# Performance work log

Hardware: AMD Instinct MI355X
Metric: run time of the kernel (lower is better)

The kernel has to match this reference:

```python
import jax, jax.numpy as jnp
import numpy as np

DIM = 1024
VOCAB = 32000
NSEQ = 32
LENGTHS = 64 - np.arange(NSEQ) // 2  # descending seq lengths 64..49 (packed seqs are length-sorted)


def setup_inputs() -> dict:
    key = jax.random.key(0)
    k1, k2, k3, k4, k5 = jax.random.split(key, 5)
    T = int(LENGTHS.max())
    batch_sizes = np.array([(LENGTHS > t).sum() for t in range(T)], dtype=np.int32)
    total = int(batch_sizes.sum())  # 1808 packed tokens
    hidden_states = jax.random.normal(k1, (total, 2 * DIM), dtype=jnp.float32)
    sentences = jax.random.randint(k2, (total,), 0, VOCAB, dtype=jnp.int32)
    weight = jax.random.normal(k3, (VOCAB, DIM), dtype=jnp.float32) * (1.0 / np.sqrt(DIM))
    fwd_bias = jax.random.normal(k4, (VOCAB,), dtype=jnp.float32) * 0.01
    bwd_bias = jax.random.normal(k5, (VOCAB,), dtype=jnp.float32) * 0.01
    return {
        "hidden_states": hidden_states,
        "weight": weight,
        "fwd_bias": fwd_bias,
        "bwd_bias": bwd_bias,
        "sentences": sentences,
        "batch_sizes": jnp.asarray(batch_sizes),
    }


def _build_indices(batch_sizes):
    # Static (host-side) index construction replicating the per-timestep Python loops.
    bs = np.asarray(batch_sizes)
    off = np.concatenate([[0], np.cumsum(bs)])  # start row of each timestep block
    T = len(bs)
    # forward: hidden at t-1 (first bs[t] rows) predicts token at t
    ctx_f = np.concatenate([off[t - 1] + np.arange(bs[t]) for t in range(1, T)])
    tgt_f = np.concatenate([off[t] + np.arange(bs[t]) for t in range(1, T)])
    # backward: hidden at i+1 predicts token at i (first bs[i+1] rows), i = T-2 .. 1
    ctx_b = np.concatenate([off[i + 1] + np.arange(bs[i + 1]) for i in range(1, T - 1)])
    tgt_b = np.concatenate([off[i] + np.arange(bs[i + 1]) for i in range(1, T - 1)])
    denom = float(2 * bs.sum() - bs[0] - bs[-1])
    return ctx_f, tgt_f, ctx_b, tgt_b, denom


def _ce_sum(h, W, b, tgt):
    # sum-reduced cross entropy: one fused GEMM over all packed rows
    logits = h @ W.T + b  # [N, V]
    lse = jax.nn.logsumexp(logits, axis=-1)  # [N]
    gold = jnp.take_along_axis(logits, tgt[:, None], axis=1)[:, 0]  # [N]
    return jnp.sum(lse - gold)


def reference(hidden_states, weight, fwd_bias, bwd_bias, sentences, batch_sizes):
    dim = hidden_states.shape[1] // 2
    ctx_f, tgt_f, ctx_b, tgt_b, denom = _build_indices(batch_sizes)
    loss_f = _ce_sum(hidden_states[ctx_f, :dim], weight, fwd_bias, sentences[tgt_f])
    loss_b = _ce_sum(hidden_states[ctx_b, dim:], weight, bwd_bias, sentences[tgt_b])
    return (loss_f + loss_b) / denom
```

## Files before the change

### kernel.cpp

```cpp
#include <hip/hip_runtime.h>
#include <hip/hip_bf16.h>
#include <stdint.h>

typedef float f32x16 __attribute__((ext_vector_type(16)));
typedef int   i32x4  __attribute__((ext_vector_type(4)));
typedef int   i32x8  __attribute__((ext_vector_type(8)));

#define LOG2E 1.4426950408889634f
#define WSCALE 16.0f
#define AS1 __attribute__((address_space(1)))
#define AS3 __attribute__((address_space(3)))


__device__ __forceinline__ uint32_t f32_to_e4m3(float x) {
    uint32_t ux = __float_as_uint(x);
    uint32_t s = (ux >> 24) & 0x80u;
    float a = __uint_as_float(ux & 0x7FFFFFFFu);
    if (a >= 448.0f) return s | 0x7Eu;
    int e = (int)((ux >> 23) & 0xFFu) - 127;
    if (e < -6) {
        int n = __float2int_rn(a * 512.0f);
        return s | (uint32_t)n;
    }
    uint32_t m = ux & 0x7FFFFFu;
    uint32_t r = (m + 0x7FFFFu + ((m >> 20) & 1u)) >> 20;
    if (r == 8u) { r = 0u; e += 1; }
    if (e > 8 || (e == 8 && r == 7u)) return s | 0x7Eu;
    return s | ((uint32_t)(e + 7) << 3) | r;
}

__device__ __forceinline__ uint32_t pack4_fp8v(float4 v, float sc) {
    return f32_to_e4m3(v.x * sc) | (f32_to_e4m3(v.y * sc) << 8) |
           (f32_to_e4m3(v.z * sc) << 16) | (f32_to_e4m3(v.w * sc) << 24);
}

__device__ __forceinline__ uint32_t pack4_fp8(const float* s, float sc) {
    return f32_to_e4m3(s[0] * sc) | (f32_to_e4m3(s[1] * sc) << 8) |
           (f32_to_e4m3(s[2] * sc) << 16) | (f32_to_e4m3(s[3] * sc) << 24);
}

__device__ __forceinline__ uint4 cvt16_fp8(const float* s, float sc) {
    uint4 r;
    r.x = pack4_fp8(s, sc);      r.y = pack4_fp8(s + 4, sc);
    r.z = pack4_fp8(s + 8, sc);  r.w = pack4_fp8(s + 12, sc);
    return r;
}

__global__ void prep_kernel(const int* __restrict__ bs, int T,
                            const int* __restrict__ sentences,
                            int* __restrict__ hdr, float* __restrict__ fhdr,
                            int* __restrict__ row_ctx, int* __restrict__ row_tok) {
    __shared__ int off[1025];
    if (threadIdx.x == 0) {
        int acc = 0; off[0] = 0;
        for (int t = 0; t < T; ++t) { acc += bs[t]; off[t + 1] = acc; }
    }
    __syncthreads();
    const int total = off[T];
    const int Nf = total - off[1];
    const int Nb = total - off[2];
    for (int t = 1; t < T; ++t) {
        int start = off[t] - off[1];
        int cnt = off[t + 1] - off[t];
        for (int p = threadIdx.x; p < cnt; p += blockDim.x) {
            row_ctx[start + p] = off[t - 1] + p;
            row_tok[start + p] = sentences[off[t] + p];
        }
    }
    for (int i = 1; i < T - 1; ++i) {
        int start = Nf + off[i + 1] - off[2];
        int cnt = off[i + 2] - off[i + 1];
        for (int p = threadIdx.x; p < cnt; p += blockDim.x) {
            row_ctx[start + p] = off[i + 1] + p;
            row_tok[start + p] = sentences[off[i] + p];
        }
    }
    if (threadIdx.x == 0) {
        hdr[0] = Nf + Nb;
        hdr[1] = Nf;
        int bs0 = off[1];
        int bsl = off[T] - off[T - 1];
        fhdr[0] = (float)(2 * total - bs0 - bsl);
    }
}

__global__ void wconv_kernel(const float* __restrict__ W,
                             uint8_t* __restrict__ Wb, int K) {
    const int p = blockIdx.x >> 3, f = blockIdx.x & 7;
    __shared__ __align__(16) char tile[2048];
    char* panel = (char*)Wb + (size_t)p * ((size_t)K << 8);
    const int tid = threadIdx.x;
    const int rloc = tid >> 4;
    const int kloc = (tid & 15) << 2;
    const int h = (kloc >> 4) & 1;
    const int l = ((kloc >> 5) << 5) | rloc;
    const int ldst = h * 1024 + l * 16 + (kloc & 15);
    const float* src = W + (size_t)(p * 256 + f * 32 + rloc) * K + kloc;
    const int NT = K >> 6;
    for (int t = 0; t < NT; ++t) {
        const float4 v = *(const float4*)(src + t * 64);
        const uint32_t pk = pack4_fp8v(v, WSCALE);
        __syncthreads();
        *(uint32_t*)(tile + ldst) = pk;
        __syncthreads();
        if (tid < 128)
            *(uint4*)(panel + (size_t)t * 16384 + f * 2048 + (tid << 4)) =
                *(const uint4*)(tile + (tid << 4));
    }
}

__global__ void gather_kernel(const float* __restrict__ hs,
                              const int* __restrict__ row_ctx,
                              const int* __restrict__ hdr,
                              uint8_t* __restrict__ Hc,
                              float* __restrict__ S, int D2, int K) {
    const int p = blockIdx.x >> 2, f = blockIdx.x & 3;
    const int M = hdr[0], Nf = hdr[1];
    if (f == 0 && threadIdx.x < 128) S[p * 128 + threadIdx.x] = 0.f;
    char* panel = (char*)Hc + (size_t)p * ((size_t)K << 7);
    const int row0 = p * 128 + f * 32;
    const int nch = (K >> 6) << 7;
    for (int c = threadIdx.x; c < nch; c += 512) {
        const int t = c >> 7, h = (c >> 6) & 1, l = c & 63;
        const int row = row0 + (l & 31);
        char* d = panel + (size_t)t * 8192 + f * 2048 + h * 1024 + l * 16;
        if (row >= M) {
            uint4 z; z.x = z.y = z.z = z.w = 0u;
            *(uint4*)d = z;
        } else {
            const int ctx = row_ctx[row];
            const int k = t * 64 + ((l >> 5) << 5) + h * 16;
            *(uint4*)d = cvt16_fp8(hs + (size_t)ctx * D2 + (row < Nf ? 0 : K) + k, 1.0f);
        }
    }
}

__device__ __forceinline__ i32x8 ld_frag(const char* base) {
    i32x4 lo = *(const i32x4*)(base);
    i32x4 hi = *(const i32x4*)(base + 1024);
    i32x8 r;
    r[0] = lo[0]; r[1] = lo[1]; r[2] = lo[2]; r[3] = lo[3];
    r[4] = hi[0]; r[5] = hi[1]; r[6] = hi[2]; r[7] = hi[3];
    return r;
}

__global__ __launch_bounds__(512, 4)
void gemm_lse(const uint8_t* __restrict__ A,
              const uint8_t* __restrict__ B,
              const float* __restrict__ fb,
              const float* __restrict__ bb,
              float* __restrict__ S,
              const int* __restrict__ hdr, int K, int MT) {
    const int M = hdr[0], Nf = hdr[1];

    const int nwg = gridDim.x, orig = blockIdx.x;
    const int q = nwg >> 3, rr = nwg & 7;
    const int xcd = orig & 7, i8 = orig >> 3;
    const int wgid = (xcd < rr ? xcd * (q + 1) : rr * (q + 1) + (xcd - rr) * q) + i8;
    const int bm = wgid % MT, bn = wgid / MT;
    if (bm * 128 >= M) return;

    __shared__ __align__(16) char lA[2][8192];
    __shared__ __align__(16) char lB[2][16384];

    const int tid = threadIdx.x, lane = tid & 63, wid = tid >> 6;
    const int wm = wid >> 2, wn = wid & 3;

    f32x16 acc00 = (f32x16)0.f, acc01 = (f32x16)0.f;
    f32x16 acc10 = (f32x16)0.f, acc11 = (f32x16)0.f;

    const char* Ap = (const char*)A + (size_t)bm * ((size_t)K << 7);
    const char* Bp = (const char*)B + (size_t)bn * ((size_t)K << 8);
    const int sd = tid << 4;
    const int ao = ((wm * 2) << 11) + (lane << 4);
    const int bo = ((wn * 2) << 11) + (lane << 4);

#define GLDS(src, dst) __builtin_amdgcn_global_load_lds(                      \
        (const AS1 uint32_t*)(src), (AS3 uint32_t*)(dst), 16, 0, 0)

#define STAGE(buf, s) do {                                                    \
    GLDS(Ap + ((size_t)(s) << 13) + sd,        lA[buf] + sd);                 \
    GLDS(Bp + ((size_t)(s) << 14) + sd,        lB[buf] + sd);                 \
    GLDS(Bp + ((size_t)(s) << 14) + 8192 + sd, lB[buf] + 8192 + sd);          \
} while (0)

#define COMPUTE(buf) do {                                                     \
    i32x8 a0 = ld_frag(lA[buf] + ao);                                         \
    i32x8 a1 = ld_frag(lA[buf] + ao + 2048);                                  \
    i32x8 b0 = ld_frag(lB[buf] + bo);                                         \
    i32x8 b1 = ld_frag(lB[buf] + bo + 2048);                                  \
    __builtin_amdgcn_s_setprio(1);                                            \
    acc00 = __builtin_amdgcn_mfma_scale_f32_32x32x64_f8f6f4(                  \
        a0, b0, acc00, 0, 0, 0, 127, 0, 127);                                 \
    acc01 = __builtin_amdgcn_mfma_scale_f32_32x32x64_f8f6f4(                  \
        a0, b1, acc01, 0, 0, 0, 127, 0, 127);                                 \
    acc10 = __builtin_amdgcn_mfma_scale_f32_32x32x64_f8f6f4(                  \
        a1, b0, acc10, 0, 0, 0, 127, 0, 127);                                 \
    acc11 = __builtin_amdgcn_mfma_scale_f32_32x32x64_f8f6f4(                  \
        a1, b1, acc11, 0, 0, 0, 127, 0, 127);                                 \
    __builtin_amdgcn_s_setprio(0);                                            \
} while (0)

#define BAR() do { __builtin_amdgcn_s_barrier(); __builtin_amdgcn_sched_barrier(0); } while (0)

    const int NT = K >> 6;

    STAGE(0, 0);
    for (int t = 0; t < NT - 1; ++t) {
        STAGE((t + 1) & 1, t + 1);
        asm volatile("s_waitcnt vmcnt(3)" ::: "memory");
        BAR();
        COMPUTE(t & 1);
        BAR();
    }
    asm volatile("s_waitcnt vmcnt(0)" ::: "memory");
    BAR();
    COMPUTE((NT - 1) & 1);

    const float k1 = LOG2E / WSCALE;
    const int v0 = bn * 256 + wn * 64 + (lane & 31);
    const float fbv0 = fb[v0] * LOG2E,      bbv0 = bb[v0] * LOG2E;
    const float fbv1 = fb[v0 + 32] * LOG2E, bbv1 = bb[v0 + 32] * LOG2E;
    const int mb0 = bm * 128 + wm * 64 + ((lane >> 5) << 2);

#define EPI(T0, T1, MB) do {                                                  \
    _Pragma("unroll")                                                         \
    for (int reg = 0; reg < 16; ++reg) {                                      \
        const int m = (MB) + (reg & 3) + ((reg >> 2) << 3);                   \
        if (m < M) {            \
            const bool isf = m < Nf;                                          \
            float ps = exp2f(fmaf(T0[reg], k1, isf ? fbv0 : bbv0))            \
                     + exp2f(fmaf(T1[reg], k1, isf ? fbv1 : bbv1));           \
            _Pragma("unroll")                                                 \
            for (int s = 1; s < 32; s <<= 1) ps += __shfl_xor(ps, s);         \
            if ((lane & 31) == 0) atomicAdd(&S[m], ps);                       \
        }                                                                     \
    }                                                                         \
} while (0)

    EPI(acc00, acc01, mb0);
    EPI(acc10, acc11, mb0 + 32);

#undef GLDS
#undef STAGE
#undef COMPUTE
#undef BAR
#undef EPI
}

__global__ void lse_naive(const float* __restrict__ hs,
                          const float* __restrict__ W,
                          const float* __restrict__ fb,
                          const float* __restrict__ bb,
                          const int* __restrict__ row_ctx,
                          const int* __restrict__ hdr,
                          float* __restrict__ S, int D2, int D, int V) {
    const int m = blockIdx.x;
    const int M = hdr[0], Nf = hdr[1];
    if (m >= M) return;
    __shared__ float hrow[2048];
    const int ctx = row_ctx[m];
    const float* h = hs + (size_t)ctx * D2 + (m < Nf ? 0 : D);
    for (int i = threadIdx.x; i < D; i += blockDim.x) hrow[i] = h[i];
    __syncthreads();
    const float* bias = (m < Nf) ? fb : bb;
    float ps = 0.f;
    for (int v = threadIdx.x; v < V; v += blockDim.x) {
        const float* w = W + (size_t)v * D;
        float dot = 0.f;
        for (int k = 0; k < D; ++k) dot = fmaf(hrow[k], w[k], dot);
        ps += exp2f((dot + bias[v]) * LOG2E);
    }
#pragma unroll
    for (int d = 1; d < 64; d <<= 1) ps += __shfl_xor(ps, d);
    __shared__ float wsum[4];
    const int wid = threadIdx.x >> 6, lane = threadIdx.x & 63;
    if (lane == 0) wsum[wid] = ps;
    __syncthreads();
    if (threadIdx.x == 0) S[m] = wsum[0] + wsum[1] + wsum[2] + wsum[3];
}

__global__ void gold_kernel(const float* __restrict__ hs,
                            const float* __restrict__ W,
                            const float* __restrict__ fb,
                            const float* __restrict__ bb,
                            const int* __restrict__ row_ctx,
                            const int* __restrict__ row_tok,
                            const int* __restrict__ hdr,
                            float* __restrict__ goldv, int D2, int D) {
    const int m = blockIdx.x;
    const int M = hdr[0];
    if (m >= M) return;
    const int Nf = hdr[1];
    const int ctx = row_ctx[m], tok = row_tok[m];
    const float4* h = (const float4*)(hs + (size_t)ctx * D2 + (m < Nf ? 0 : D));
    const float4* w = (const float4*)(W + (size_t)tok * D);
    float s = 0.f;
    for (int i = threadIdx.x; i < D / 4; i += blockDim.x) {
        float4 a = h[i], b = w[i];
        s += a.x * b.x + a.y * b.y + a.z * b.z + a.w * b.w;
    }
#pragma unroll
    for (int d = 1; d < 64; d <<= 1) s += __shfl_xor(s, d);
    __shared__ float wsum[4];
    const int wid = threadIdx.x >> 6, lane = threadIdx.x & 63;
    if (lane == 0) wsum[wid] = s;
    __syncthreads();
    if (threadIdx.x == 0) {
        float tot = wsum[0] + wsum[1] + wsum[2] + wsum[3];
        tot += (m < Nf ? fb[tok] : bb[tok]);
        goldv[m] = tot;
    }
}

__global__ void final_kernel(const float* __restrict__ S,
                             const float* __restrict__ goldv,
                             const int* __restrict__ hdr,
                             const float* __restrict__ fhdr,
                             float* __restrict__ out) {
    const int M = hdr[0];
    float s = 0.f;
    for (int m = threadIdx.x; m < M; m += blockDim.x)
        s += logf(S[m]) - goldv[m];
#pragma unroll
    for (int d = 1; d < 64; d <<= 1) s += __shfl_xor(s, d);
    __shared__ float wsum[4];
    const int wid = threadIdx.x >> 6, lane = threadIdx.x & 63;
    if (lane == 0) wsum[wid] = s;
    __syncthreads();
    if (threadIdx.x == 0)
        out[0] = (wsum[0] + wsum[1] + wsum[2] + wsum[3]) / fhdr[0];
}

extern "C" void kernel_launch(void* const* d_in, const int* in_sizes, int n_in,
                              void* d_out, int out_size, void* d_ws, size_t ws_size,
                              hipStream_t stream) {
    const float* hs  = (const float*)d_in[0];
    const float* W   = (const float*)d_in[1];
    const float* fb  = (const float*)d_in[2];
    const float* bb  = (const float*)d_in[3];
    const int* sent  = (const int*)d_in[4];
    const int* bs    = (const int*)d_in[5];
    const int total  = in_sizes[4];
    const int T      = in_sizes[5];
    const int V      = in_sizes[2];
    const int D      = in_sizes[1] / V;
    const int D2     = in_sizes[0] / total;
    const int Mcap   = ((2 * total) + 127) & ~127;
    const int MT     = Mcap / 128;
    const int NN     = V / 256;

    char* p = (char*)d_ws;
    int*   hdr     = (int*)p;            p += 256;
    float* fhdr    = (float*)p;          p += 256;
    int*   row_ctx = (int*)p;            p += (size_t)Mcap * 4;
    int*   row_tok = (int*)p;            p += (size_t)Mcap * 4;
    float* S       = (float*)p;          p += (size_t)Mcap * 4;
    float* goldv   = (float*)p;          p += (size_t)Mcap * 4;
    uint8_t* Hc    = (uint8_t*)p;        p += (size_t)Mcap * D;
    uint8_t* Wb    = (uint8_t*)p;
    const size_t need_wb = (size_t)(p - (char*)d_ws) + (size_t)V * D;

    prep_kernel<<<1, 256, 0, stream>>>(bs, T, sent, hdr, fhdr, row_ctx, row_tok);

    if (ws_size >= need_wb) {
        gather_kernel<<<MT * 4, 512, 0, stream>>>(hs, row_ctx, hdr, Hc, S, D2, D);
        wconv_kernel<<<(V / 256) * 8, 512, 0, stream>>>(W, Wb, D);
        gemm_lse<<<NN * MT, 512, 0, stream>>>(Hc, Wb, fb, bb, S, hdr, D, MT);
    } else {
        lse_naive<<<Mcap, 256, 0, stream>>>(hs, W, fb, bb, row_ctx, hdr, S, D2, D, V);
    }

    gold_kernel<<<Mcap, 256, 0, stream>>>(hs, W, fb, bb, row_ctx, row_tok, hdr, goldv, D2, D);
    final_kernel<<<1, 256, 0, stream>>>(S, goldv, hdr, fhdr, (float*)d_out);
}
```

Baseline: 298.3 us.

## Drop LDS staging in FP8 GEMM; load MFMA fragments directly into registers

Measured after the change: 283.5 us. 5.0% less time.

```diff
diff --git a/kernel.cpp b/kernel.cpp
--- a/kernel.cpp
+++ b/kernel.cpp
@@ -8,8 +8,6 @@
 
 #define LOG2E 1.4426950408889634f
 #define WSCALE 16.0f
-#define AS1 __attribute__((address_space(1)))
-#define AS3 __attribute__((address_space(3)))
 
 
 __device__ __forceinline__ uint32_t f32_to_e4m3(float x) {
@@ -135,16 +133,7 @@
     }
 }
 
-__device__ __forceinline__ i32x8 ld_frag(const char* base) {
-    i32x4 lo = *(const i32x4*)(base);
-    i32x4 hi = *(const i32x4*)(base + 1024);
-    i32x8 r;
-    r[0] = lo[0]; r[1] = lo[1]; r[2] = lo[2]; r[3] = lo[3];
-    r[4] = hi[0]; r[5] = hi[1]; r[6] = hi[2]; r[7] = hi[3];
-    return r;
-}
-
-__global__ __launch_bounds__(512, 4)
+__global__ __launch_bounds__(256, 3)
 void gemm_lse(const uint8_t* __restrict__ A,
               const uint8_t* __restrict__ B,
               const float* __restrict__ fb,
@@ -160,65 +149,66 @@
     const int bm = wgid % MT, bn = wgid / MT;
     if (bm * 128 >= M) return;
 
-    __shared__ __align__(16) char lA[2][8192];
-    __shared__ __align__(16) char lB[2][16384];
-
     const int tid = threadIdx.x, lane = tid & 63, wid = tid >> 6;
-    const int wm = wid >> 2, wn = wid & 3;
+    const int wm = wid >> 1, wn = wid & 1;
 
     f32x16 acc00 = (f32x16)0.f, acc01 = (f32x16)0.f;
     f32x16 acc10 = (f32x16)0.f, acc11 = (f32x16)0.f;
 
-    const char* Ap = (const char*)A + (size_t)bm * ((size_t)K << 7);
-    const char* Bp = (const char*)B + (size_t)bn * ((size_t)K << 8);
-    const int sd = tid << 4;
-    const int ao = ((wm * 2) << 11) + (lane << 4);
-    const int bo = ((wn * 2) << 11) + (lane << 4);
-
-#define GLDS(src, dst) __builtin_amdgcn_global_load_lds(                      \
-        (const AS1 uint32_t*)(src), (AS3 uint32_t*)(dst), 16, 0, 0)
-
-#define STAGE(buf, s) do {                                                    \
-    GLDS(Ap + ((size_t)(s) << 13) + sd,        lA[buf] + sd);                 \
-    GLDS(Bp + ((size_t)(s) << 14) + sd,        lB[buf] + sd);                 \
-    GLDS(Bp + ((size_t)(s) << 14) + 8192 + sd, lB[buf] + 8192 + sd);          \
+    const char* pa = (const char*)A + (size_t)bm * ((size_t)K << 7)
+                     + (wm << 12) + (lane << 4);
+    const char* pb = (const char*)B + (size_t)(bn >> 1) * ((size_t)K << 8)
+                     + ((bn & 1) << 13) + (wn << 12) + (lane << 4);
+
+    i32x4 xa0l, xa0h, xa1l, xa1h, xb0l, xb0h, xb1l, xb1h;
+    i32x4 ya0l, ya0h, ya1l, ya1h, yb0l, yb0h, yb1l, yb1h;
+
+#define LOADS(P, t) do {                                                      \
+    const char* _a = pa + (size_t)(t) * 8192;                                 \
+    const char* _b = pb + (size_t)(t) * 16384;                                \
+    P##a0l = *(const i32x4*)(_a);          P##a0h = *(const i32x4*)(_a + 1024); \
+    P##a1l = *(const i32x4*)(_a + 2048);   P##a1h = *(const i32x4*)(_a + 3072); \
+    P##b0l = *(const i32x4*)(_b);          P##b0h = *(const i32x4*)(_b + 1024); \
+    P##b1l = *(const i32x4*)(_b + 2048);   P##b1h = *(const i32x4*)(_b + 3072); \
 } while (0)
 
-#define COMPUTE(buf) do {                                                     \
-    i32x8 a0 = ld_frag(lA[buf] + ao);                                         \
-    i32x8 a1 = ld_frag(lA[buf] + ao + 2048);                                  \
-    i32x8 b0 = ld_frag(lB[buf] + bo);                                         \
-    i32x8 b1 = ld_frag(lB[buf] + bo + 2048);                                  \
-    __builtin_amdgcn_s_setprio(1);                                            \
+#define CAT8(lo, hi) __builtin_shufflevector(lo, hi, 0, 1, 2, 3, 4, 5, 6, 7)
+
+#define COMP(P) do {                                                          \
+    const i32x8 A0 = CAT8(P##a0l, P##a0h);                                    \
+    const i32x8 A1 = CAT8(P##a1l, P##a1h);                                    \
+    const i32x8 B0 = CAT8(P##b0l, P##b0h);                                    \
+    const i32x8 B1 = CAT8(P##b1l, P##b1h);                                    \
     acc00 = __builtin_amdgcn_mfma_scale_f32_32x32x64_f8f6f4(                  \
-        a0, b0, acc00, 0, 0, 0, 127, 0, 127);                                 \
+        A0, B0, acc00, 0, 0, 0, 127, 0, 127);                                 \
     acc01 = __builtin_amdgcn_mfma_scale_f32_32x32x64_f8f6f4(                  \
-        a0, b1, acc01, 0, 0, 0, 127, 0, 127);                                 \
+        A0, B1, acc01, 0, 0, 0, 127, 0, 127);                                 \
     acc10 = __builtin_amdgcn_mfma_scale_f32_32x32x64_f8f6f4(                  \
-        a1, b0, acc10, 0, 0, 0, 127, 0, 127);                                 \
+        A1, B0, acc10, 0, 0, 0, 127, 0, 127);                                 \
     acc11 = __builtin_amdgcn_mfma_scale_f32_32x32x64_f8f6f4(                  \
-        a1, b1, acc11, 0, 0, 0, 127, 0, 127);                                 \
-    __builtin_amdgcn_s_setprio(0);                                            \
+        A1, B1, acc11, 0, 0, 0, 127, 0, 127);                                 \
 } while (0)
 
-#define BAR() do { __builtin_amdgcn_s_barrier(); __builtin_amdgcn_sched_barrier(0); } while (0)
-
     const int NT = K >> 6;
 
-    STAGE(0, 0);
-    for (int t = 0; t < NT - 1; ++t) {
-        STAGE((t + 1) & 1, t + 1);
-        asm volatile("s_waitcnt vmcnt(3)" ::: "memory");
-        BAR();
-        COMPUTE(t & 1);
-        BAR();
-    }
-    asm volatile("s_waitcnt vmcnt(0)" ::: "memory");
-    BAR();
-    COMPUTE((NT - 1) & 1);
+    LOADS(x, 0);
+    int t = 0;
+    for (; t + 2 < NT; t += 2) {
+        LOADS(y, t + 1);
+        COMP(x);
+        LOADS(x, t + 2);
+        COMP(y);
+    }
+    if ((NT & 1) == 0) {
+        LOADS(y, t + 1);
+        COMP(x);
+        COMP(y);
+    } else {
+        COMP(x);
+    }
 
     const float k1 = LOG2E / WSCALE;
-    const int v0 = bn * 256 + wn * 64 + (lane & 31);
+    const int v0 = bn * 128 + wn * 64 + (lane & 31);
     const float fbv0 = fb[v0] * LOG2E,      bbv0 = bb[v0] * LOG2E;
     const float fbv1 = fb[v0 + 32] * LOG2E, bbv1 = bb[v0 + 32] * LOG2E;
     const int mb0 = bm * 128 + wm * 64 + ((lane >> 5) << 2);
@@ -227,7 +217,7 @@
     _Pragma("unroll")                                                         \
     for (int reg = 0; reg < 16; ++reg) {                                      \
         const int m = (MB) + (reg & 3) + ((reg >> 2) << 3);                   \
-        if (m < M) {            \
+        if (m < M) {           \
             const bool isf = m < Nf;                                          \
             float ps = exp2f(fmaf(T0[reg], k1, isf ? fbv0 : bbv0))            \
                      + exp2f(fmaf(T1[reg], k1, isf ? fbv1 : bbv1));           \
@@ -241,10 +231,9 @@
     EPI(acc00, acc01, mb0);
     EPI(acc10, acc11, mb0 + 32);
 
-#undef GLDS
-#undef STAGE
-#undef COMPUTE
-#undef BAR
+#undef LOADS
+#undef CAT8
+#undef COMP
 #undef EPI
 }
 
@@ -348,7 +337,7 @@
     const int D2     = in_sizes[0] / total;
     const int Mcap   = ((2 * total) + 127) & ~127;
     const int MT     = Mcap / 128;
-    const int NN     = V / 256;
+    const int NN2    = V / 128;
 
     char* p = (char*)d_ws;
     int*   hdr     = (int*)p;            p += 256;
@@ -366,7 +355,7 @@
     if (ws_size >= need_wb) {
         gather_kernel<<<MT * 4, 512, 0, stream>>>(hs, row_ctx, hdr, Hc, S, D2, D);
         wconv_kernel<<<(V / 256) * 8, 512, 0, stream>>>(W, Wb, D);
-        gemm_lse<<<NN * MT, 512, 0, stream>>>(Hc, Wb, fb, bb, S, hdr, D, MT);
+        gemm_lse<<<NN2 * MT, 256, 0, stream>>>(Hc, Wb, fb, bb, S, hdr, D, MT);
     } else {
         lse_naive<<<Mcap, 256, 0, stream>>>(hs, W, fb, bb, row_ctx, hdr, S, D2, D, V);
     }
```
